# Optimization experiments

Measured on AMD Instinct MI355X. Metric: run time of the kernel, lower is better.

## Reference

```python
import jax, jax.numpy as jnp
import numpy as np

KERNELS = (2, 3, 6, 7)
ALPHA = 2.0
DT = 1.0  # time=1.0, step_size=1.0 -> one RK4 (3/8 rule) step, as torchdiffeq 'rk4'


def _conv(x, w, b):
    # x: [B,C,N,L], w: [O,I,1,k] -> valid conv over time axis
    y = jax.lax.conv_general_dilated(x, w, (1, 1), 'VALID',
                                     dimension_numbers=('NCHW', 'OIHW', 'NCHW'))
    return y + b[None, :, None, None]


def _inception(x, ws, bs):
    outs = [_conv(x, w, b) for w, b in zip(ws, bs)]
    L = outs[-1].shape[-1]  # shortest output (largest kernel=7)
    return jnp.concatenate([o[..., -L:] for o in outs], axis=1)


def _norm_adj(adj):
    A = adj + jnp.eye(adj.shape[0], dtype=adj.dtype)
    dinv = A.sum(1) ** -0.5
    return dinv[:, None] * A * dinv[None, :]  # D^-1/2 (A+I) D^-1/2


def _cgp(x, A_norm, mw, mb):
    f = lambda y: 0.5 * ALPHA * (jnp.einsum('ncwl,vw->ncvl', y, A_norm) - y)
    k1 = f(x)
    y2 = x + (DT / 3.0) * k1
    k2 = f(y2)
    y3 = x + DT * (k2 - k1 / 3.0)
    k3 = f(y3)
    y4 = x + DT * (k1 - k2 + k3)
    k4 = f(y4)
    yf = x + (DT / 8.0) * (k1 + 3.0 * (k2 + k3) + k4)
    # odefunc.out collects the state at each of the 4 f-evals, plus final state
    cat = jnp.concatenate([x, y2, y3, y4, yf], axis=1)  # [B, 5C, N, L]
    return _conv(cat, mw, mb)


def setup_inputs() -> dict:
    key = jax.random.key(0)
    B, C, N, T = 8, 64, 512, 64
    cq = C // 4
    ks = jax.random.split(key, 24)
    d = {
        'x': jax.random.normal(ks[0], (B, C, N, T), dtype=jnp.float32),
        'adj': jax.random.uniform(ks[1], (N, N), dtype=jnp.float32),
    }
    i = 2
    for branch in ('i1', 'i2'):
        for j, k in enumerate(KERNELS):
            d[f'{branch}w{j}'] = 0.1 * jax.random.normal(ks[i], (cq, C, 1, k), dtype=jnp.float32); i += 1
            d[f'{branch}b{j}'] = 0.1 * jax.random.normal(ks[i], (cq,), dtype=jnp.float32); i += 1
    d['m1w'] = 0.1 * jax.random.normal(ks[i], (C, 5 * C, 1, 1), dtype=jnp.float32); i += 1
    d['m1b'] = 0.1 * jax.random.normal(ks[i], (C,), dtype=jnp.float32); i += 1
    d['m2w'] = 0.1 * jax.random.normal(ks[i], (C, 5 * C, 1, 1), dtype=jnp.float32); i += 1
    d['m2b'] = 0.1 * jax.random.normal(ks[i], (C,), dtype=jnp.float32)
    return d


def reference(x, adj,
              i1w0, i1b0, i1w1, i1b1, i1w2, i1b2, i1w3, i1b3,
              i2w0, i2b0, i2w1, i2b1, i2w2, i2b2, i2w3, i2b3,
              m1w, m1b, m2w, m2b):
    T = x.shape[-1]  # receptive_field
    filt = jnp.tanh(_inception(x, (i1w0, i1w1, i1w2, i1w3), (i1b0, i1b1, i1b2, i1b3)))
    gate = jax.nn.sigmoid(_inception(x, (i2w0, i2w1, i2w2, i2w3), (i2b0, i2b1, i2b2, i2b3)))
    h = filt * gate  # dropout is identity in eval mode
    An = _norm_adj(adj)
    AnT = _norm_adj(adj.T)
    h = _cgp(h, An, m1w, m1b) + _cgp(h, AnT, m2w, m2b)
    pad = T - h.shape[-1]
    return jnp.pad(h, ((0, 0), (0, 0), (0, 0), (pad, 0)))
```

## Files before the change

kernel.cpp:

```cpp
#include <hip/hip_runtime.h>
#include <math.h>

#define NN 512
#define BB 8
#define CC 64
#define TT 64
#define LL 58
#define CL (CC*LL)
#define BCL (BB*CC*LL)
#define SZ ((size_t)NN*BCL)

typedef _Float16 half8 __attribute__((ext_vector_type(8)));
typedef _Float16 half4 __attribute__((ext_vector_type(4)));
typedef float f32x4 __attribute__((ext_vector_type(4)));

__global__ __launch_bounds__(64) void prep_adj(const float* __restrict__ adj,
                                               float* __restrict__ dinv1,
                                               float* __restrict__ dinv2){
  int v = blockIdx.x;
  int lane = threadIdx.x;
  float rs = 0.f, cs = 0.f;
  for (int w = lane; w < NN; w += 64){
    rs += adj[v*NN + w];
    cs += adj[w*NN + v];
  }
  for (int off = 32; off > 0; off >>= 1){
    rs += __shfl_down(rs, off);
    cs += __shfl_down(cs, off);
  }
  if (lane == 0){
    dinv1[v] = 1.f / sqrtf(rs + 1.f);
    dinv2[v] = 1.f / sqrtf(cs + 1.f);
  }
}

__global__ __launch_bounds__(256) void build_norm(const float* __restrict__ adj,
                                                  const float* __restrict__ dinv1,
                                                  const float* __restrict__ dinv2,
                                                  _Float16* __restrict__ An,
                                                  _Float16* __restrict__ AnT){
  int v = blockIdx.x;
  float d1v = dinv1[v], d2v = dinv2[v];
  for (int w = threadIdx.x; w < NN; w += 256){
    float diag = (v == w) ? 1.f : 0.f;
    An[v*NN + w]  = (_Float16)(d1v * (adj[v*NN + w] + diag) * dinv1[w] - diag);
    AnT[v*NN + w] = (_Float16)(d2v * (adj[w*NN + v] + diag) * dinv2[w] - diag);
  }
}

__global__ __launch_bounds__(256) void u_prep(const float* __restrict__ W1,
                                              const float* __restrict__ W2,
                                              _Float16* __restrict__ U1,
                                              _Float16* __restrict__ U2){
  const float coef[5][5] = {
    {1.f, 1.f, 1.f, 1.f, 1.f},
    {0.f, 1.f/3.f, 2.f/3.f, 1.f, 1.f},
    {0.f, 0.f, 1.f/3.f, 1.f/3.f, 0.5f},
    {0.f, 0.f, 0.f, 1.f/3.f, 1.f/6.f},
    {0.f, 0.f, 0.f, 0.f, 1.f/24.f}};
  int idx = blockIdx.x*256 + threadIdx.x;
  int o = idx / 320, rem = idx - o*320;
  int d = rem >> 6, c = rem & 63;
  float a1 = 0.f, a2 = 0.f;
  #pragma unroll
  for (int s = 0; s < 5; ++s){
    float cf = coef[d][s];
    a1 += cf * W1[o*320 + s*64 + c];
    a2 += cf * W2[o*320 + s*64 + c];
  }
  U1[idx] = (_Float16)a1;
  U2[idx] = (_Float16)a2;
}

__global__ __launch_bounds__(448) void wfg_prep(
    const float* __restrict__ w10, const float* __restrict__ w11,
    const float* __restrict__ w12, const float* __restrict__ w13,
    const float* __restrict__ w20, const float* __restrict__ w21,
    const float* __restrict__ w22, const float* __restrict__ w23,
    const float* __restrict__ b10, const float* __restrict__ b11,
    const float* __restrict__ b12, const float* __restrict__ b13,
    const float* __restrict__ b20, const float* __restrict__ b21,
    const float* __restrict__ b22, const float* __restrict__ b23,
    _Float16* __restrict__ WfG, float* __restrict__ biasFG){
  int r = blockIdx.x;
  int t = threadIdx.x;
  int qp = t >> 6, ic = t & 63;
  int gate = r >> 6;
  int j = (r >> 4) & 3;
  int oc = r & 15;
  const int kjs[4] = {2, 3, 6, 7};
  int kj = kjs[j];
  const float* wsel = gate ? ((j==0)?w20:(j==1)?w21:(j==2)?w22:w23)
                           : ((j==0)?w10:(j==1)?w11:(j==2)?w12:w13);
  int off = 7 - kj;
  float val = (qp >= off) ? wsel[(oc*64 + ic)*kj + (qp - off)] : 0.f;
  WfG[(size_t)r*448 + t] = (_Float16)val;
  if (t == 0){
    const float* bsel = gate ? ((j==0)?b20:(j==1)?b21:(j==2)?b22:b23)
                             : ((j==0)?b10:(j==1)?b11:(j==2)?b12:b13);
    biasFG[r] = bsel[oc];
  }
}

__global__ __launch_bounds__(256) void xt_prep(const float* __restrict__ x,
                                               _Float16* __restrict__ xTg){
  __shared__ float T[64][65];
  int n = blockIdx.x;
  int b = blockIdx.y;
  int tid = threadIdx.x;
  #pragma unroll
  for (int r = 0; r < 4; ++r){
    int f = tid + r*256;
    int ic = f >> 4, t4 = f & 15;
    float4 v = *(const float4*)&x[(((size_t)(b*64 + ic))*512 + n)*64 + t4*4];
    T[ic][t4*4+0] = v.x; T[ic][t4*4+1] = v.y;
    T[ic][t4*4+2] = v.z; T[ic][t4*4+3] = v.w;
  }
  __syncthreads();
  #pragma unroll
  for (int r = 0; r < 2; ++r){
    int f = tid + r*256;
    int t = f >> 3, ch = f & 7;
    half8 hv;
    #pragma unroll
    for (int q2 = 0; q2 < 8; ++q2) hv[q2] = (_Float16)T[ch*8 + q2][t];
    *(half8*)&xTg[(((size_t)(b*64 + t))*512 + n)*64 + ch*8] = hv;
  }
}

__global__ __launch_bounds__(256, 3) void inception_mfma(
    const _Float16* __restrict__ xTg,
    const _Float16* __restrict__ WfG,
    const float* __restrict__ biasFG,
    _Float16* __restrict__ S_h){
  __shared__ _Float16 X[13*32*64];
  int nt = blockIdx.x;
  int lt = blockIdx.y;
  int b  = blockIdx.z;
  int n0 = nt*32, l0 = lt*7;
  int tid = threadIdx.x;

  int sch = tid & 7, sn = (tid >> 3) & 31;
  #pragma unroll
  for (int r = 0; r < 13; ++r){
    int t = l0 + r;
    half8 v = {};
    if (t < 64)
      v = *(const half8*)&xTg[(((size_t)(b*64 + t))*512 + n0 + sn)*64 + sch*8];
    *(half8*)&X[(size_t)(r*256 + sn*8 + (sch ^ (sn & 7)))*8] = v;
  }

  int w = tid >> 6, lane = tid & 63;
  int m = lane & 15, kg = lane >> 4;

  half8 wF[14], wG[14];
  const _Float16* wb = WfG + (size_t)(w*16 + m)*448 + kg*8;
  #pragma unroll
  for (int s = 0; s < 14; ++s){
    wF[s] = *(const half8*)(wb + s*32);
    wG[s] = *(const half8*)(wb + (size_t)64*448 + s*32);
  }
  f32x4 bF = *(const f32x4*)&biasFG[w*16 + kg*4];
  f32x4 bG = *(const f32x4*)&biasFG[64 + w*16 + kg*4];

  __syncthreads();

  for (int ll = 0; ll < 7; ++ll){
    f32x4 aF0 = {}, aF1 = {}, aG0 = {}, aG1 = {};
    #pragma unroll
    for (int s = 0; s < 14; ++s){
      int t = ll + (s >> 1);
      int c0 = (s & 1)*4 + kg;
      half8 b0 = *(half8*)&X[(size_t)(t*256 + m*8        + (c0 ^ (m & 7)))*8];
      half8 b1 = *(half8*)&X[(size_t)(t*256 + (16+m)*8   + (c0 ^ (m & 7)))*8];
      aF0 = __builtin_amdgcn_mfma_f32_16x16x32_f16(wF[s], b0, aF0, 0, 0, 0);
      aG0 = __builtin_amdgcn_mfma_f32_16x16x32_f16(wG[s], b0, aG0, 0, 0, 0);
      aF1 = __builtin_amdgcn_mfma_f32_16x16x32_f16(wF[s], b1, aF1, 0, 0, 0);
      aG1 = __builtin_amdgcn_mfma_f32_16x16x32_f16(wG[s], b1, aG1, 0, 0, 0);
    }
    int l = l0 + ll;
    if (l < LL){
      #pragma unroll
      for (int rr = 0; rr < 4; ++rr){
        int c = w*16 + kg*4 + rr;
        float F0 = aF0[rr] + bF[rr];
        float G0 = aG0[rr] + bG[rr];
        float F1 = aF1[rr] + bF[rr];
        float G1 = aG1[rr] + bG[rr];
        float h0 = (2.f*__builtin_amdgcn_rcpf(1.f + __expf(-2.f*F0)) - 1.f)
                 * __builtin_amdgcn_rcpf(1.f + __expf(-G0));
        float h1 = (2.f*__builtin_amdgcn_rcpf(1.f + __expf(-2.f*F1)) - 1.f)
                 * __builtin_amdgcn_rcpf(1.f + __expf(-G1));
        size_t base = ((size_t)(b*64 + c)*LL + l)*NN + n0;
        S_h[base + m]      = (_Float16)h0;
        S_h[base + 16 + m] = (_Float16)h1;
      }
    }
  }
}

__device__ __forceinline__ void gll16(const _Float16* g, _Float16* l){
  __builtin_amdgcn_global_load_lds(
      (const __attribute__((address_space(1))) unsigned int*)g,
      (__attribute__((address_space(3))) unsigned int*)l, 16, 0, 0);
}
#define BAR() asm volatile("s_barrier" ::: "memory")

__global__ __launch_bounds__(256, 2) void gemm_z2(
    int nx,
    const _Float16* __restrict__ A0, const _Float16* __restrict__ B0,
    _Float16* __restrict__ O0,
    const _Float16* __restrict__ A1, const _Float16* __restrict__ B1,
    _Float16* __restrict__ O1){
  __shared__ _Float16 L[32768];

  int bid = blockIdx.x;
  int q8 = gridDim.x >> 3;
  int virt = (bid & 7)*q8 + (bid >> 3);
  int y = virt & 1;
  int pair = virt >> 1;
  int x = pair % nx;
  int z = pair / nx;

  const _Float16* __restrict__ A = z ? A1 : A0;
  const _Float16* __restrict__ B = z ? B1 : B0;
  _Float16* __restrict__ O = z ? O1 : O0;

  const int m0 = x * 128;
  const int v0 = y * 256;
  const int tid = threadIdx.x;
  const int ww = tid >> 6;
  const int lane = tid & 63;
  const int lr = lane & 15;
  const int kg = lane >> 4;
  const int wvq = ww & 1;
  const int wmq = ww >> 1;

  const int srow = lane >> 2;
  const int gch  = ((lane & 3) - ((lane >> 3) & 3)) & 3;
  const _Float16* gAb = A + (size_t)(v0 + ww*64 + srow)*NN + gch*8;
  const _Float16* gBb = B + (size_t)(m0 + ww*32 + srow)*NN + gch*8;

  #define STAGE(buf, kt)                                                    \
    { char* lA_ = (char*)L + (buf)*24576 + ww*4096;                         \
      char* lB_ = (char*)L + (buf)*24576 + 16384 + ww*2048;                 \
      const _Float16* gA_ = gAb + (kt)*32;                                  \
      const _Float16* gB_ = gBb + (kt)*32;                                  \
      _Pragma("unroll")                                                     \
      for (int s_ = 0; s_ < 4; ++s_)                                        \
        gll16(gA_ + (size_t)s_*16*NN, (_Float16*)(lA_ + s_*1024));          \
      _Pragma("unroll")                                                     \
      for (int s_ = 0; s_ < 2; ++s_)                                        \
        gll16(gB_ + (size_t)s_*16*NN, (_Float16*)(lB_ + s_*1024)); }

  const int slot = (kg + (lr >> 1)) & 3;
  const int aOff = (wvq*128 + lr)*64 + slot*16;
  const int bOff = 16384 + (wmq*64 + lr)*64 + slot*16;

  half8 af[8], bf[4];
  f32x4 acc[8][4] = {};

  STAGE(0, 0)
  STAGE(1, 1)
  asm volatile("s_waitcnt vmcnt(6)" ::: "memory");
  BAR();

  #pragma unroll
  for (int kt = 0; kt < 16; ++kt){
    const int buf = kt & 1;
    char* lb = (char*)L + buf*24576;
    #pragma unroll
    for (int i = 0; i < 8; ++i) af[i] = *(const half8*)(lb + aOff + i*1024);
    #pragma unroll
    for (int j = 0; j < 4; ++j) bf[j] = *(const half8*)(lb + bOff + j*1024);
    asm volatile("s_waitcnt lgkmcnt(0)" ::: "memory");
    BAR();
    if (kt + 2 < 16) STAGE(buf, kt + 2)

    __builtin_amdgcn_s_setprio(1);
    #pragma unroll
    for (int i = 0; i < 8; ++i)
      #pragma unroll
      for (int j = 0; j < 4; ++j)
        acc[i][j] = __builtin_amdgcn_mfma_f32_16x16x32_f16(af[i], bf[j], acc[i][j], 0, 0, 0);
    __builtin_amdgcn_s_setprio(0);

    if (kt < 14){
      asm volatile("s_waitcnt vmcnt(6)" ::: "memory");
      BAR();
    } else if (kt == 14){
      asm volatile("s_waitcnt vmcnt(0)" ::: "memory");
      BAR();
    }
  }
  #undef STAGE

  char* Lw = (char*)L + ww*16384;
  #pragma unroll
  for (int j = 0; j < 4; ++j){
    int row = j*16 + lr;
    #pragma unroll
    for (int i = 0; i < 8; ++i){
      int c = (i*4 + kg) ^ ((lr & 7)*4);
      half4 oq;
      #pragma unroll
      for (int rr = 0; rr < 4; ++rr) oq[rr] = (_Float16)acc[i][j][rr];
      *(half4*)(Lw + row*256 + c*8) = oq;
    }
  }
  #pragma unroll
  for (int s = 0; s < 16; ++s){
    int row = s*4 + kg;
    int cc = (2*lr) ^ ((row & 7)*4);
    half8 hv = *(const half8*)(Lw + row*256 + cc*8);
    *(half8*)&O[(size_t)(m0 + wmq*64 + row)*NN + v0 + wvq*128 + lr*8] = hv;
  }
}

template<int PASS>
__global__ __launch_bounds__(256, 3) void combine_mfma(
    const _Float16* __restrict__ Sh, const _Float16* __restrict__ S2,
    const _Float16* __restrict__ S3, const _Float16* __restrict__ S4,
    const _Float16* __restrict__ Sf,
    const _Float16* __restrict__ Wc,
    const float* __restrict__ bias,
    _Float16* __restrict__ tmp){
  __shared__ __align__(16) _Float16 Xt[256*64];
  __shared__ float Bsh[64];
  int v0 = blockIdx.x * 256;
  int l  = blockIdx.y;
  int b  = blockIdx.z;
  int tid = threadIdx.x;
  int w = tid >> 6, lane = tid & 63;
  int lr = lane & 15, kg = lane >> 4;

  if (tid < 64) Bsh[tid] = bias[tid];

  const int c0  = ((tid >> 3) & 7) * 8;
  const int lv0 = (tid & 7) * 8 + w * 64;
  const int wslot = (c0 >> 3) ^ (((lv0 >> 3) & 1) << 2);
  const int rx = ((lr >> 3) & 1) << 2;

  const _Float16* Sarr[5] = {Sh, S2, S3, S4, Sf};
  f32x4 acc[4][4] = {};

  for (int kt = 0; kt < 5; ++kt){
    const _Float16* S = Sarr[kt];
    unsigned xr[8][4];
    const _Float16* gbase = &S[((size_t)(b*64 + c0)*58 + l)*512 + v0 + lv0];
    #pragma unroll
    for (int r = 0; r < 8; ++r)
      *(uint4*)xr[r] = *(const uint4*)(gbase + (size_t)r*58*512);

    __syncthreads();

    #pragma unroll
    for (int q = 0; q < 8; ++q){
      const unsigned sel = (q & 1) ? 0x07060302u : 0x05040100u;
      const int d2 = q >> 1;
      uint4 y;
      y.x = __builtin_amdgcn_perm(xr[1][d2], xr[0][d2], sel);
      y.y = __builtin_amdgcn_perm(xr[3][d2], xr[2][d2], sel);
      y.z = __builtin_amdgcn_perm(xr[5][d2], xr[4][d2], sel);
      y.w = __builtin_amdgcn_perm(xr[7][d2], xr[6][d2], sel);
      *(uint4*)((char*)Xt + (lv0 + q)*128 + wslot*16) = y;
    }

    half8 aW[2][4];
    #pragma unroll
    for (int ks = 0; ks < 2; ++ks)
      #pragma unroll
      for (int jj = 0; jj < 4; ++jj)
        aW[ks][jj] = *(const half8*)&Wc[(size_t)(jj*16 + lr)*320
                                        + kt*64 + ks*32 + kg*8];

    __syncthreads();

    #pragma unroll
    for (int ks = 0; ks < 2; ++ks){
      #pragma unroll
      for (int vt = 0; vt < 4; ++vt){
        half8 bf = *(const half8*)((char*)Xt + (w*64 + vt*16 + lr)*128
                                   + ((ks*4 + kg) ^ rx)*16);
        #pragma unroll
        for (int jj = 0; jj < 4; ++jj)
          acc[vt][jj] = __builtin_amdgcn_mfma_f32_16x16x32_f16(
              aW[ks][jj], bf, acc[vt][jj], 0, 0, 0);
      }
    }
  }

  size_t rowbase = ((size_t)b*58 + l)*64;
  #pragma unroll
  for (int jj = 0; jj < 4; ++jj){
    #pragma unroll
    for (int rr = 0; rr < 4; ++rr){
      int o = jj*16 + kg*4 + rr;
      float bv = Bsh[o];
      size_t obase = (rowbase + o)*512 + v0 + w*64 + lr;
      #pragma unroll
      for (int vt = 0; vt < 4; ++vt){
        float val = acc[vt][jj][rr] + bv;
        size_t addr = obase + vt*16;
        if (PASS == 0) tmp[addr] = (_Float16)val;
        else           tmp[addr] = (_Float16)((float)tmp[addr] + val);
      }
    }
  }
}

__global__ __launch_bounds__(256) void untranspose(const _Float16* __restrict__ tmp,
                                                   float* __restrict__ out){
  __shared__ float T[58][65];
  int o = blockIdx.x;
  int b = blockIdx.y;
  int v0 = blockIdx.z * 64;
  int t = threadIdx.x;
  for (int idx = t; idx < 58*64; idx += 256){
    int lr = idx >> 6, vv = idx & 63;
    T[lr][vv] = (float)tmp[((size_t)(b*58 + lr)*64 + o)*NN + v0 + vv];
  }
  __syncthreads();
  #pragma unroll
  for (int i = 0; i < 16; ++i){
    int c = t + i*256;
    int vv = c >> 6, tt = c & 63;
    float val = (tt < 6) ? 0.f : T[tt - 6][vv];
    out[((size_t)(b*64 + o)*NN + v0 + vv)*TT + tt] = val;
  }
}

extern "C" void kernel_launch(void* const* d_in, const int* in_sizes, int n_in,
                              void* d_out, int out_size, void* d_ws, size_t ws_size,
                              hipStream_t stream){
  const float* x   = (const float*)d_in[0];
  const float* adj = (const float*)d_in[1];
  const float* w1[4] = {(const float*)d_in[2],  (const float*)d_in[4],
                        (const float*)d_in[6],  (const float*)d_in[8]};
  const float* b1[4] = {(const float*)d_in[3],  (const float*)d_in[5],
                        (const float*)d_in[7],  (const float*)d_in[9]};
  const float* w2[4] = {(const float*)d_in[10], (const float*)d_in[12],
                        (const float*)d_in[14], (const float*)d_in[16]};
  const float* b2[4] = {(const float*)d_in[11], (const float*)d_in[13],
                        (const float*)d_in[15], (const float*)d_in[17]};
  const float* m1w = (const float*)d_in[18];
  const float* m1b = (const float*)d_in[19];
  const float* m2w = (const float*)d_in[20];
  const float* m2b = (const float*)d_in[21];

  char* wsb = (char*)d_ws;
  float* dinv1 = (float*)(wsb);
  float* dinv2 = (float*)(wsb + 2048);
  _Float16* U1  = (_Float16*)(wsb + 4096);
  _Float16* U2  = (_Float16*)(wsb + 4096 + 40960);
  _Float16* Mn  = (_Float16*)(wsb + 167936);
  _Float16* MnT = (_Float16*)(wsb + 167936 + 524288);
  size_t sbytes = SZ * 2;
  char* sbase = wsb + 1216512;
  _Float16* S_h = (_Float16*)(sbase);
  _Float16* S2  = (_Float16*)(sbase + sbytes);
  _Float16* S3  = (_Float16*)(sbase + 2*sbytes);
  _Float16* S4  = (_Float16*)(sbase + 3*sbytes);
  _Float16* S5  = (_Float16*)(sbase + 4*sbytes);
  _Float16* tmp = (_Float16*)(sbase + 5*sbytes);
  _Float16* xTg = S2;
  _Float16* WfG = (_Float16*)(sbase + 6*sbytes);
  float* biasFG = (float*)(sbase + 6*sbytes + 114688);
  _Float16* M2  = (_Float16*)(sbase + 6*sbytes + 131072);
  _Float16* MT2 = (_Float16*)(sbase + 6*sbytes + 131072 + 524288);
  float* out = (float*)d_out;

  prep_adj<<<NN, 64, 0, stream>>>(adj, dinv1, dinv2);
  build_norm<<<NN, 256, 0, stream>>>(adj, dinv1, dinv2, Mn, MnT);
  gemm_z2<<<16, 256, 0, stream>>>(4, MnT, Mn, M2, Mn, MnT, MT2);
  u_prep<<<80, 256, 0, stream>>>(m1w, m2w, U1, U2);
  wfg_prep<<<128, 448, 0, stream>>>(
      w1[0],w1[1],w1[2],w1[3], w2[0],w2[1],w2[2],w2[3],
      b1[0],b1[1],b1[2],b1[3], b2[0],b2[1],b2[2],b2[3], WfG, biasFG);
  xt_prep<<<dim3(NN, BB), 256, 0, stream>>>(x, xTg);
  inception_mfma<<<dim3(16, 9, 8), 256, 0, stream>>>(xTg, WfG, biasFG, S_h);

  dim3 gc(2, LL, BB);
  for (int pass = 0; pass < 2; ++pass){
    const _Float16* Mp  = pass ? MnT : Mn;
    const _Float16* Mp2 = pass ? MT2 : M2;
    gemm_z2<<<928, 256, 0, stream>>>(232, Mp, S_h, S2, Mp2, S_h, S3);
    gemm_z2<<<928, 256, 0, stream>>>(232, Mp2, S2, S4, Mp2, S3, S5);
    if (pass == 0)
      combine_mfma<0><<<gc, 256, 0, stream>>>(S_h, S2, S3, S4, S5, U1, m1b, tmp);
    else
      combine_mfma<1><<<gc, 256, 0, stream>>>(S_h, S2, S3, S4, S5, U2, m2b, tmp);
  }
  untranspose<<<dim3(64, 8, 8), 256, 0, stream>>>(tmp, out);
}
```

Baseline: 460.7 us.

## Restructure inception MFMA loop to reuse LDS tiles across output timesteps

Reorders the inception convolution so each LDS row of X is loaded once per channel half and applied to all 7 output timesteps, using 28 accumulator registers instead of reloading X per output step. Weights are now loaded in two halves of 7 instead of all 14 at once. This cuts LDS reads roughly sevenfold but raises accumulator register use, so occupancy is lowered from 3 to 2 waves per SIMD via launch bounds.

```diff
diff --git a/kernel.cpp b/kernel.cpp
--- a/kernel.cpp
+++ b/kernel.cpp
@@ -128,7 +128,7 @@
   }
 }
 
-__global__ __launch_bounds__(256, 3) void inception_mfma(
+__global__ __launch_bounds__(256, 2) void inception_mfma(
     const _Float16* __restrict__ xTg,
     const _Float16* __restrict__ WfG,
     const float* __restrict__ biasFG,
@@ -153,40 +153,51 @@
   int w = tid >> 6, lane = tid & 63;
   int m = lane & 15, kg = lane >> 4;
 
-  half8 wF[14], wG[14];
+  f32x4 aF0[7] = {}, aG0[7] = {}, aF1[7] = {}, aG1[7] = {};
+
+  __syncthreads();
+
   const _Float16* wb = WfG + (size_t)(w*16 + m)*448 + kg*8;
-  #pragma unroll
-  for (int s = 0; s < 14; ++s){
-    wF[s] = *(const half8*)(wb + s*32);
-    wG[s] = *(const half8*)(wb + (size_t)64*448 + s*32);
-  }
+  for (int ch = 0; ch < 2; ++ch){
+    half8 wF7[7], wG7[7];
+    #pragma unroll
+    for (int d = 0; d < 7; ++d){
+      wF7[d] = *(const half8*)(wb + (2*d + ch)*32);
+      wG7[d] = *(const half8*)(wb + (size_t)64*448 + (2*d + ch)*32);
+    }
+    int c0 = ch*4 + kg;
+    int xoff = m*64 + (c0 ^ (m & 7))*8;
+    #pragma unroll
+    for (int td = 0; td < 13; ++td){
+      half8 b0 = *(const half8*)&X[td*2048 + xoff];
+      half8 b1 = *(const half8*)&X[td*2048 + 1024 + xoff];
+      #pragma unroll
+      for (int d = 0; d < 7; ++d){
+        if (d <= td && d >= td - 6){
+          int ll = td - d;
+          aF0[ll] = __builtin_amdgcn_mfma_f32_16x16x32_f16(wF7[d], b0, aF0[ll], 0, 0, 0);
+          aG0[ll] = __builtin_amdgcn_mfma_f32_16x16x32_f16(wG7[d], b0, aG0[ll], 0, 0, 0);
+          aF1[ll] = __builtin_amdgcn_mfma_f32_16x16x32_f16(wF7[d], b1, aF1[ll], 0, 0, 0);
+          aG1[ll] = __builtin_amdgcn_mfma_f32_16x16x32_f16(wG7[d], b1, aG1[ll], 0, 0, 0);
+        }
+      }
+    }
+  }
+
   f32x4 bF = *(const f32x4*)&biasFG[w*16 + kg*4];
   f32x4 bG = *(const f32x4*)&biasFG[64 + w*16 + kg*4];
 
-  __syncthreads();
-
+  #pragma unroll
   for (int ll = 0; ll < 7; ++ll){
-    f32x4 aF0 = {}, aF1 = {}, aG0 = {}, aG1 = {};
-    #pragma unroll
-    for (int s = 0; s < 14; ++s){
-      int t = ll + (s >> 1);
-      int c0 = (s & 1)*4 + kg;
-      half8 b0 = *(half8*)&X[(size_t)(t*256 + m*8        + (c0 ^ (m & 7)))*8];
-      half8 b1 = *(half8*)&X[(size_t)(t*256 + (16+m)*8   + (c0 ^ (m & 7)))*8];
-      aF0 = __builtin_amdgcn_mfma_f32_16x16x32_f16(wF[s], b0, aF0, 0, 0, 0);
-      aG0 = __builtin_amdgcn_mfma_f32_16x16x32_f16(wG[s], b0, aG0, 0, 0, 0);
-      aF1 = __builtin_amdgcn_mfma_f32_16x16x32_f16(wF[s], b1, aF1, 0, 0, 0);
-      aG1 = __builtin_amdgcn_mfma_f32_16x16x32_f16(wG[s], b1, aG1, 0, 0, 0);
-    }
     int l = l0 + ll;
     if (l < LL){
       #pragma unroll
       for (int rr = 0; rr < 4; ++rr){
         int c = w*16 + kg*4 + rr;
-        float F0 = aF0[rr] + bF[rr];
-        float G0 = aG0[rr] + bG[rr];
-        float F1 = aF1[rr] + bF[rr];
-        float G1 = aG1[rr] + bG[rr];
+        float F0 = aF0[ll][rr] + bF[rr];
+        float G0 = aG0[ll][rr] + bG[rr];
+        float F1 = aF1[ll][rr] + bF[rr];
+        float G1 = aG1[ll][rr] + bG[rr];
         float h0 = (2.f*__builtin_amdgcn_rcpf(1.f + __expf(-2.f*F0)) - 1.f)
                  * __builtin_amdgcn_rcpf(1.f + __expf(-G0));
         float h1 = (2.f*__builtin_amdgcn_rcpf(1.f + __expf(-2.f*F1)) - 1.f)
```

Measured after the change: 473.5 us. 2.8% more time.
